# Kernel tuning notes

Measured on AMD Instinct MI355X. Metric: run time of the kernel, lower is better.

## Reference

```python
import jax, jax.numpy as jnp
import numpy as np

HIDDEN = 256
N_HEADS = 4
HEAD_DIM = HIDDEN // N_HEADS
SCALE = float(np.sqrt(HEAD_DIM))


def setup_inputs() -> dict:
    key = jax.random.key(0)
    ks = jax.random.split(key, 10)
    B, NQ, NKV = 2, 4096, 4096
    s = 1.0 / np.sqrt(HIDDEN)
    inp = {
        "query": jax.random.normal(ks[0], (B, NQ, HIDDEN), dtype=jnp.float32),
        "key_value": jax.random.normal(ks[1], (B, NKV, HIDDEN), dtype=jnp.float32),
        "kv_mask": jnp.ones((B, NKV), dtype=jnp.int32),
        "Wq": jax.random.uniform(ks[2], (HIDDEN, HIDDEN), jnp.float32, -s, s),
        "bq": jnp.zeros((HIDDEN,), jnp.float32),
        "Wk": jax.random.uniform(ks[3], (HIDDEN, HIDDEN), jnp.float32, -s, s),
        "bk": jnp.zeros((HIDDEN,), jnp.float32),
        "Wv": jax.random.uniform(ks[4], (HIDDEN, HIDDEN), jnp.float32, -s, s),
        "bv": jnp.zeros((HIDDEN,), jnp.float32),
        "Wo": jax.random.uniform(ks[5], (HIDDEN, HIDDEN), jnp.float32, -s, s),
        "bo": jnp.zeros((HIDDEN,), jnp.float32),
    }
    return inp


def reference(query, key_value, kv_mask, Wq, bq, Wk, bk, Wv, bv, Wo, bo):
    B, NQ, D = query.shape
    NKV = key_value.shape[1]
    # projections; reshape to (B, H, S, Dh)
    q = (query @ Wq + bq).reshape(B, NQ, N_HEADS, HEAD_DIM).transpose(0, 2, 1, 3)
    k = (key_value @ Wk + bk).reshape(B, NKV, N_HEADS, HEAD_DIM).transpose(0, 2, 1, 3)
    v = (key_value @ Wv + bv).reshape(B, NKV, N_HEADS, HEAD_DIM).transpose(0, 2, 1, 3)
    # scores: (B, H, NQ, NKV)
    attn = jnp.einsum("bhqd,bhkd->bhqk", q, k) / SCALE
    mask = (kv_mask != 0)[:, None, None, :]  # (B,1,1,NKV)
    attn = jnp.where(mask, attn, -jnp.inf)
    attn = jax.nn.softmax(attn, axis=-1)
    # dropout is identity in eval mode (reference is deterministic)
    out = jnp.einsum("bhqk,bhkd->bhqd", attn, v)
    out = out.transpose(0, 2, 1, 3).reshape(B, NQ, D)
    return out @ Wo + bo
```

## Files before the change

kernel.cpp:

```cpp
#include <hip/hip_runtime.h>
#include <hip/hip_bf16.h>
#include <math.h>

#define HID   256
#define NHEADS  4
#define HDIM   64
#define SEQ  4096
#define BATCH   2
#define MTOK (BATCH * SEQ)
#define LOG2E 1.44269504088896340736f
#define MFIX  8.0f

typedef short bf16x8 __attribute__((ext_vector_type(8)));
typedef float f32x4  __attribute__((ext_vector_type(4)));

__device__ __forceinline__ unsigned short f2b(float f) {
  union { float f; unsigned u; } v; v.f = f;
  return (unsigned short)((v.u + 0x7FFFu + ((v.u >> 16) & 1u)) >> 16);
}
__device__ __forceinline__ unsigned pkb(float a, float b) {
  __hip_bfloat162 h = __float22bfloat162_rn(make_float2(a, b));
  union { __hip_bfloat162 h; unsigned u; } v; v.h = h;
  return v.u;
}
__device__ __forceinline__ float exp2_(float x) {
#if __has_builtin(__builtin_amdgcn_exp2f)
  return __builtin_amdgcn_exp2f(x);
#else
  return exp2f(x);
#endif
}

__global__ __launch_bounds__(256)
void cast_wt(const float* __restrict__ W0, const float* __restrict__ W1,
             const float* __restrict__ W2, const float* __restrict__ W3,
             unsigned short* __restrict__ Wt) {
  __shared__ float t[64][65];
  const float* Ws[4] = {W0, W1, W2, W3};
  const float scl[4] = {0.125f * LOG2E, 1.f, 1.f, 1.f};
  const int wsel = blockIdx.y;
  const float* W = Ws[wsel];
  const float s = scl[wsel];
  unsigned short* O = Wt + (size_t)wsel * HID * HID;
  const int kt = (blockIdx.x & 3) * 64, nt = (blockIdx.x >> 2) * 64;
  const int tid = threadIdx.x;
#pragma unroll
  for (int p = 0; p < 4; ++p) {
    int i = p * 256 + tid;
    int r = i >> 4, c4 = (i & 15) * 4;
    *(float4*)&t[r][c4] = *(const float4*)&W[(size_t)(kt + r) * HID + nt + c4];
  }
  __syncthreads();
#pragma unroll
  for (int p = 0; p < 4; ++p) {
    int i = p * 256 + tid;
    int rn = i >> 4, ck = (i & 15) * 4;
    ushort4 o;
    o.x = f2b(t[ck + 0][rn] * s);
    o.y = f2b(t[ck + 1][rn] * s);
    o.z = f2b(t[ck + 2][rn] * s);
    o.w = f2b(t[ck + 3][rn] * s);
    *(ushort4*)&O[(size_t)(nt + rn) * HID + kt + ck] = o;
  }
}

__global__ __launch_bounds__(256)
void gemm_qkv(const float* __restrict__ query, const float* __restrict__ keyv,
              const unsigned short* __restrict__ wts,
              const float* __restrict__ bq, const float* __restrict__ bk,
              const float* __restrict__ bv,
              unsigned short* qp, unsigned short* kp, unsigned short* vtp) {
  __shared__ __align__(16) unsigned short As[2][64][136];
  __shared__ __align__(16) unsigned short Bs[64][136];
  float (*L)[68] = (float (*)[68])&Bs[0][0];

  const int tid = threadIdx.x;
  const int w = tid >> 6, lane = tid & 63, lq = lane & 15, quad = lane >> 4;
  const int wm = w & 1, wn = w >> 1;
  const int z = blockIdx.y;
  const int m0 = blockIdx.x * 64;

  const float* A = (z == 0) ? query : keyv;
  const unsigned short* Bt = wts + (size_t)z * HID * HID;
  const float* bias = (z == 0) ? bq : ((z == 1) ? bk : bv);
  const float bscale = (z == 0) ? 0.125f * LOG2E : 1.0f;

#pragma unroll
  for (int p = 0; p < 16; ++p) {
    int i = p * 256 + tid;
    int r = i >> 6, c4 = (i & 63) * 4;
    float4 f4 = *(const float4*)&A[(size_t)(m0 + r) * HID + c4];
    unsigned lo = pkb(f4.x, f4.y), hi = pkb(f4.z, f4.w);
    *(uint2*)&As[c4 >> 7][r][c4 & 127] = make_uint2(lo, hi);
  }
  __syncthreads();

  for (int n = 0; n < 4; ++n) {
    const int n0 = n * 64;
    f32x4 acc[2][2];
#pragma unroll
    for (int i = 0; i < 2; ++i)
#pragma unroll
      for (int j = 0; j < 2; ++j) acc[i][j] = (f32x4){0.f, 0.f, 0.f, 0.f};

#pragma unroll
    for (int kt = 0; kt < 2; ++kt) {
#pragma unroll
      for (int p = 0; p < 4; ++p) {
        int i = p * 256 + tid;
        int r = i >> 4, c8 = (i & 15) * 8;
        *(uint4*)&Bs[r][c8] =
            *(const uint4*)&Bt[(size_t)(n0 + r) * HID + kt * 128 + c8];
      }
      __syncthreads();
#pragma unroll
      for (int ks = 0; ks < 4; ++ks) {
        bf16x8 a0 = *(const bf16x8*)&As[kt][wm * 32 + lq][ks * 32 + quad * 8];
        bf16x8 a1 = *(const bf16x8*)&As[kt][wm * 32 + 16 + lq][ks * 32 + quad * 8];
        bf16x8 b0 = *(const bf16x8*)&Bs[wn * 32 + lq][ks * 32 + quad * 8];
        bf16x8 b1 = *(const bf16x8*)&Bs[wn * 32 + 16 + lq][ks * 32 + quad * 8];
        acc[0][0] = __builtin_amdgcn_mfma_f32_16x16x32_bf16(a0, b0, acc[0][0], 0, 0, 0);
        acc[0][1] = __builtin_amdgcn_mfma_f32_16x16x32_bf16(a0, b1, acc[0][1], 0, 0, 0);
        acc[1][0] = __builtin_amdgcn_mfma_f32_16x16x32_bf16(a1, b0, acc[1][0], 0, 0, 0);
        acc[1][1] = __builtin_amdgcn_mfma_f32_16x16x32_bf16(a1, b1, acc[1][1], 0, 0, 0);
      }
      __syncthreads();
    }

#pragma unroll
    for (int ni = 0; ni < 2; ++ni) {
      const float bv = bias[n0 + wn * 32 + ni * 16 + lq] * bscale;
#pragma unroll
      for (int mi = 0; mi < 2; ++mi)
#pragma unroll
        for (int r = 0; r < 4; ++r)
          L[wm * 32 + mi * 16 + quad * 4 + r][wn * 32 + ni * 16 + lq] =
              acc[mi][ni][r] + bv;
    }
    __syncthreads();

    if (z == 2) {
      const int nn = tid >> 2, mb4 = (tid & 3) * 16;
      __align__(16) unsigned short tmp[16];
#pragma unroll
      for (int j = 0; j < 16; ++j) {
        int p = mb4 + j;
        int k = ((p & 3) << 4) + (p >> 2);
        tmp[j] = f2b(L[k][nn]);
      }
      *(uint4*)&vtp[(size_t)(n0 + nn) * MTOK + m0 + mb4]     = *(uint4*)&tmp[0];
      *(uint4*)&vtp[(size_t)(n0 + nn) * MTOK + m0 + mb4 + 8] = *(uint4*)&tmp[8];
    } else {
      unsigned short* Y = (z == 0) ? qp : kp;
      const int r = tid >> 2, cb = (tid & 3) * 16;
      __align__(16) unsigned short tmp[16];
#pragma unroll
      for (int j = 0; j < 4; ++j) {
        float4 v4 = *(const float4*)&L[r][cb + j * 4];
        *(uint2*)&tmp[j * 4] = make_uint2(pkb(v4.x, v4.y), pkb(v4.z, v4.w));
      }
      *(uint4*)&Y[(size_t)(m0 + r) * HID + n0 + cb]     = *(uint4*)&tmp[0];
      *(uint4*)&Y[(size_t)(m0 + r) * HID + n0 + cb + 8] = *(uint4*)&tmp[8];
    }
    __syncthreads();
  }
}

__global__ __launch_bounds__(256)
void gemm_out(const unsigned short* __restrict__ ao,
              const unsigned short* __restrict__ wot,
              const float* __restrict__ bo, float* __restrict__ out) {
  __shared__ __align__(16) unsigned short As[64][136];
  __shared__ __align__(16) unsigned short Bs[64][136];
  float (*L)[68] = (float (*)[68])&As[0][0];

  const int tid = threadIdx.x;
  const int w = tid >> 6, lane = tid & 63, lq = lane & 15, quad = lane >> 4;
  const int wm = w & 1, wn = w >> 1;
  const int m0 = blockIdx.y * 64, n0 = blockIdx.x * 64;

  f32x4 acc[2][2];
#pragma unroll
  for (int i = 0; i < 2; ++i)
#pragma unroll
    for (int j = 0; j < 2; ++j) acc[i][j] = (f32x4){0.f, 0.f, 0.f, 0.f};

#pragma unroll
  for (int kt = 0; kt < 2; ++kt) {
    const int k0 = kt * 128;
#pragma unroll
    for (int p = 0; p < 4; ++p) {
      int i = p * 256 + tid;
      int r = i >> 4, c8 = (i & 15) * 8;
      *(uint4*)&As[r][c8] = *(const uint4*)&ao[(size_t)(m0 + r) * HID + k0 + c8];
      *(uint4*)&Bs[r][c8] = *(const uint4*)&wot[(size_t)(n0 + r) * HID + k0 + c8];
    }
    __syncthreads();
#pragma unroll
    for (int ks = 0; ks < 4; ++ks) {
      bf16x8 a0 = *(const bf16x8*)&As[wm * 32 + lq][ks * 32 + quad * 8];
      bf16x8 a1 = *(const bf16x8*)&As[wm * 32 + 16 + lq][ks * 32 + quad * 8];
      bf16x8 b0 = *(const bf16x8*)&Bs[wn * 32 + lq][ks * 32 + quad * 8];
      bf16x8 b1 = *(const bf16x8*)&Bs[wn * 32 + 16 + lq][ks * 32 + quad * 8];
      acc[0][0] = __builtin_amdgcn_mfma_f32_16x16x32_bf16(a0, b0, acc[0][0], 0, 0, 0);
      acc[0][1] = __builtin_amdgcn_mfma_f32_16x16x32_bf16(a0, b1, acc[0][1], 0, 0, 0);
      acc[1][0] = __builtin_amdgcn_mfma_f32_16x16x32_bf16(a1, b0, acc[1][0], 0, 0, 0);
      acc[1][1] = __builtin_amdgcn_mfma_f32_16x16x32_bf16(a1, b1, acc[1][1], 0, 0, 0);
    }
    __syncthreads();
  }

#pragma unroll
  for (int ni = 0; ni < 2; ++ni) {
    const float bv = bo[n0 + wn * 32 + ni * 16 + lq];
#pragma unroll
    for (int mi = 0; mi < 2; ++mi)
#pragma unroll
      for (int r = 0; r < 4; ++r)
        L[wm * 32 + mi * 16 + quad * 4 + r][wn * 32 + ni * 16 + lq] =
            acc[mi][ni][r] + bv;
  }
  __syncthreads();

  const int r = tid >> 2, cb = (tid & 3) * 16;
#pragma unroll
  for (int j = 0; j < 4; ++j) {
    float4 v4 = *(const float4*)&L[r][cb + j * 4];
    *(float4*)&out[(size_t)(m0 + r) * HID + n0 + cb + j * 4] = v4;
  }
}

__global__ __launch_bounds__(512, 2)
void flash_attn_mfma(const unsigned short* __restrict__ Qp,
                     const unsigned short* __restrict__ Kp,
                     const unsigned short* __restrict__ Vtp,
                     const int* __restrict__ mask,
                     unsigned short* __restrict__ Ao) {
  __shared__ __align__(16) unsigned short Ks[128][72];
  __shared__ __align__(16) unsigned short Vt[64][136];
  __shared__ __align__(16) unsigned short Ps[8][16][72];
  __shared__ float mb[128];

  const int tid = threadIdx.x;
  const int w = tid >> 6, lane = tid & 63, lq = lane & 15, quad = lane >> 4;
  const int bh = blockIdx.x;
  const int b = bh >> 2, h = bh & 3;
  const int q0 = blockIdx.y * 128;
  const int qbase = b * SEQ + q0, kvbase = b * SEQ, coff = h * HDIM;

  bf16x8 qf0, qf1;
  {
    const unsigned short* qr = &Qp[(size_t)(qbase + w * 16 + lq) * HID + coff + quad * 8];
    qf0 = *(const bf16x8*)&qr[0];
    qf1 = *(const bf16x8*)&qr[32];
  }

  const short oneb = (short)0x3F80;
  const bf16x8 ones = {oneb, oneb, oneb, oneb, oneb, oneb, oneb, oneb};

  f32x4 o[4], ls;
#pragma unroll
  for (int c = 0; c < 4; ++c) o[c] = (f32x4){0.f, 0.f, 0.f, 0.f};
  ls = (f32x4){0.f, 0.f, 0.f, 0.f};

  const int NT = SEQ / 128;
  for (int t = 0; t < NT; ++t) {
    const int k0 = t * 128;
#pragma unroll
    for (int p = 0; p < 2; ++p) {
      int idx = p * 512 + tid;
      int rk = idx >> 3, ck = (idx & 7) * 8;
      uint4 k4 = *(const uint4*)&Kp[(size_t)(kvbase + k0 + rk) * HID + coff + ck];
      int rv = idx >> 4, cv = (idx & 15) * 8;
      uint4 v4 = *(const uint4*)&Vtp[(size_t)(coff + rv) * MTOK + kvbase + k0 + cv];
      *(uint4*)&Ks[rk][ck] = k4;
      *(uint4*)&Vt[rv][cv] = v4;
    }
    if (tid < 128) mb[tid] = mask[kvbase + k0 + tid] ? -MFIX : -1e30f;
    __syncthreads();

    f32x4 sc[8];
#pragma unroll
    for (int c = 0; c < 8; ++c) {
      sc[c] = (f32x4){0.f, 0.f, 0.f, 0.f};
      bf16x8 kb0 = *(const bf16x8*)&Ks[c * 16 + lq][quad * 8];
      bf16x8 kb1 = *(const bf16x8*)&Ks[c * 16 + lq][32 + quad * 8];
      sc[c] = __builtin_amdgcn_mfma_f32_16x16x32_bf16(qf0, kb0, sc[c], 0, 0, 0);
      sc[c] = __builtin_amdgcn_mfma_f32_16x16x32_bf16(qf1, kb1, sc[c], 0, 0, 0);
    }
    float mbias[8];
#pragma unroll
    for (int c = 0; c < 8; ++c) mbias[c] = mb[c * 16 + lq];

#pragma unroll
    for (int hh = 0; hh < 2; ++hh) {
#pragma unroll
      for (int r = 0; r < 4; ++r) {
        const int row = quad * 4 + r;
        unsigned a0 = pkb(exp2_(sc[hh * 4 + 0][r] + mbias[hh * 4 + 0]),
                          exp2_(sc[hh * 4 + 1][r] + mbias[hh * 4 + 1]));
        unsigned a1 = pkb(exp2_(sc[hh * 4 + 2][r] + mbias[hh * 4 + 2]),
                          exp2_(sc[hh * 4 + 3][r] + mbias[hh * 4 + 3]));
        *(uint2*)&Ps[w][row][lq * 4] = make_uint2(a0, a1);
      }
#pragma unroll
      for (int i = 0; i < 2; ++i) {
        bf16x8 pa = *(const bf16x8*)&Ps[w][lq][i * 32 + quad * 8];
        ls = __builtin_amdgcn_mfma_f32_16x16x32_bf16(pa, ones, ls, 0, 0, 0);
#pragma unroll
        for (int c = 0; c < 4; ++c) {
          bf16x8 vb = *(const bf16x8*)&Vt[c * 16 + lq][hh * 64 + i * 32 + quad * 8];
          o[c] = __builtin_amdgcn_mfma_f32_16x16x32_bf16(pa, vb, o[c], 0, 0, 0);
        }
      }
    }
    __syncthreads();
  }

#pragma unroll
  for (int r = 0; r < 4; ++r) {
    float inv = 1.f / ls[r];
    const size_t row = (size_t)(qbase + w * 16 + quad * 4 + r);
#pragma unroll
    for (int c = 0; c < 4; ++c)
      Ao[row * HID + coff + c * 16 + lq] = f2b(o[c][r] * inv);
  }
}

extern "C" void kernel_launch(void* const* d_in, const int* in_sizes, int n_in,
                              void* d_out, int out_size, void* d_ws, size_t ws_size,
                              hipStream_t stream) {
  const float* query = (const float*)d_in[0];
  const float* keyv  = (const float*)d_in[1];
  const int*   mask  = (const int*)d_in[2];
  const float* Wq = (const float*)d_in[3];
  const float* bq = (const float*)d_in[4];
  const float* Wk = (const float*)d_in[5];
  const float* bk = (const float*)d_in[6];
  const float* Wv = (const float*)d_in[7];
  const float* bv = (const float*)d_in[8];
  const float* Wo = (const float*)d_in[9];
  const float* bo = (const float*)d_in[10];
  float* out = (float*)d_out;

  unsigned short* wts = (unsigned short*)d_ws;
  unsigned short* qp  = wts + (size_t)4 * HID * HID;
  unsigned short* kp  = qp  + (size_t)MTOK * HID;
  unsigned short* vtp = kp  + (size_t)MTOK * HID;
  unsigned short* ao  = vtp + (size_t)MTOK * HID;

  const unsigned short* wo_t = wts + 3 * HID * HID;

  dim3 blk(256);
  hipLaunchKernelGGL(cast_wt, dim3(16, 4), blk, 0, stream, Wq, Wk, Wv, Wo, wts);

  dim3 qkvgrid(MTOK / 64, 3);
  hipLaunchKernelGGL(gemm_qkv, qkvgrid, blk, 0, stream,
                     query, keyv, wts, bq, bk, bv, qp, kp, vtp);

  dim3 fgrid(BATCH * NHEADS, SEQ / 128);
  hipLaunchKernelGGL(flash_attn_mfma, fgrid, dim3(512), 0, stream,
                     qp, kp, vtp, mask, ao);

  dim3 ogrid(HID / 64, MTOK / 64);
  hipLaunchKernelGGL(gemm_out, ogrid, blk, 0, stream, ao, wo_t, bo, out);
}
```

Before: 175.9 us.

## Double-buffer K/V tiles in LDS with register prefetch in flash attention

Adds two LDS buffers for K, V^T and the mask bias. The next tile is loaded into registers at the start of each iteration and written to the alternate buffer after compute, so global-load latency overlaps the MFMA work and one barrier per iteration is removed. In exchange, LDS use roughly doubles, register pressure rises, and launch bounds drop to one block per SM, which may reduce occupancy.

```diff
diff --git a/kernel.cpp b/kernel.cpp
--- a/kernel.cpp
+++ b/kernel.cpp
@@ -230,16 +230,16 @@
   }
 }
 
-__global__ __launch_bounds__(512, 2)
+__global__ __launch_bounds__(512, 1)
 void flash_attn_mfma(const unsigned short* __restrict__ Qp,
                      const unsigned short* __restrict__ Kp,
                      const unsigned short* __restrict__ Vtp,
                      const int* __restrict__ mask,
                      unsigned short* __restrict__ Ao) {
-  __shared__ __align__(16) unsigned short Ks[128][72];
-  __shared__ __align__(16) unsigned short Vt[64][136];
+  __shared__ __align__(16) unsigned short Ks[2][128][72];
+  __shared__ __align__(16) unsigned short Vt[2][64][136];
   __shared__ __align__(16) unsigned short Ps[8][16][72];
-  __shared__ float mb[128];
+  __shared__ float mb[2][128];
 
   const int tid = threadIdx.x;
   const int w = tid >> 6, lane = tid & 63, lq = lane & 15, quad = lane >> 4;
@@ -248,6 +248,11 @@
   const int q0 = blockIdx.y * 128;
   const int qbase = b * SEQ + q0, kvbase = b * SEQ, coff = h * HDIM;
 
+  const int rk0 = tid >> 3,          ck0 = (tid & 7) * 8;
+  const int rk1 = (512 + tid) >> 3,  ck1 = ((512 + tid) & 7) * 8;
+  const int rv0 = tid >> 4,          cv0 = (tid & 15) * 8;
+  const int rv1 = (512 + tid) >> 4,  cv1 = ((512 + tid) & 15) * 8;
+
   bf16x8 qf0, qf1;
   {
     const unsigned short* qr = &Qp[(size_t)(qbase + w * 16 + lq) * HID + coff + quad * 8];
@@ -263,34 +268,47 @@
   for (int c = 0; c < 4; ++c) o[c] = (f32x4){0.f, 0.f, 0.f, 0.f};
   ls = (f32x4){0.f, 0.f, 0.f, 0.f};
 
+  {
+    *(uint4*)&Ks[0][rk0][ck0] =
+        *(const uint4*)&Kp[(size_t)(kvbase + rk0) * HID + coff + ck0];
+    *(uint4*)&Ks[0][rk1][ck1] =
+        *(const uint4*)&Kp[(size_t)(kvbase + rk1) * HID + coff + ck1];
+    *(uint4*)&Vt[0][rv0][cv0] =
+        *(const uint4*)&Vtp[(size_t)(coff + rv0) * MTOK + kvbase + cv0];
+    *(uint4*)&Vt[0][rv1][cv1] =
+        *(const uint4*)&Vtp[(size_t)(coff + rv1) * MTOK + kvbase + cv1];
+    if (tid < 128) mb[0][tid] = mask[kvbase + tid] ? -MFIX : -1e30f;
+  }
+  __syncthreads();
+
   const int NT = SEQ / 128;
   for (int t = 0; t < NT; ++t) {
-    const int k0 = t * 128;
-#pragma unroll
-    for (int p = 0; p < 2; ++p) {
-      int idx = p * 512 + tid;
-      int rk = idx >> 3, ck = (idx & 7) * 8;
-      uint4 k4 = *(const uint4*)&Kp[(size_t)(kvbase + k0 + rk) * HID + coff + ck];
-      int rv = idx >> 4, cv = (idx & 15) * 8;
-      uint4 v4 = *(const uint4*)&Vtp[(size_t)(coff + rv) * MTOK + kvbase + k0 + cv];
-      *(uint4*)&Ks[rk][ck] = k4;
-      *(uint4*)&Vt[rv][cv] = v4;
-    }
-    if (tid < 128) mb[tid] = mask[kvbase + k0 + tid] ? -MFIX : -1e30f;
-    __syncthreads();
+    const int cur = t & 1, nxt = cur ^ 1;
+    const bool pf = (t + 1 < NT);
+
+    uint4 kA, kB, vA, vB;
+    float mbr = 0.f;
+    if (pf) {
+      const int k0n = (t + 1) * 128;
+      kA = *(const uint4*)&Kp[(size_t)(kvbase + k0n + rk0) * HID + coff + ck0];
+      kB = *(const uint4*)&Kp[(size_t)(kvbase + k0n + rk1) * HID + coff + ck1];
+      vA = *(const uint4*)&Vtp[(size_t)(coff + rv0) * MTOK + kvbase + k0n + cv0];
+      vB = *(const uint4*)&Vtp[(size_t)(coff + rv1) * MTOK + kvbase + k0n + cv1];
+      if (tid < 128) mbr = mask[kvbase + k0n + tid] ? -MFIX : -1e30f;
+    }
 
     f32x4 sc[8];
 #pragma unroll
     for (int c = 0; c < 8; ++c) {
       sc[c] = (f32x4){0.f, 0.f, 0.f, 0.f};
-      bf16x8 kb0 = *(const bf16x8*)&Ks[c * 16 + lq][quad * 8];
-      bf16x8 kb1 = *(const bf16x8*)&Ks[c * 16 + lq][32 + quad * 8];
+      bf16x8 kb0 = *(const bf16x8*)&Ks[cur][c * 16 + lq][quad * 8];
+      bf16x8 kb1 = *(const bf16x8*)&Ks[cur][c * 16 + lq][32 + quad * 8];
       sc[c] = __builtin_amdgcn_mfma_f32_16x16x32_bf16(qf0, kb0, sc[c], 0, 0, 0);
       sc[c] = __builtin_amdgcn_mfma_f32_16x16x32_bf16(qf1, kb1, sc[c], 0, 0, 0);
     }
     float mbias[8];
 #pragma unroll
-    for (int c = 0; c < 8; ++c) mbias[c] = mb[c * 16 + lq];
+    for (int c = 0; c < 8; ++c) mbias[c] = mb[cur][c * 16 + lq];
 
 #pragma unroll
     for (int hh = 0; hh < 2; ++hh) {
@@ -309,10 +327,18 @@
         ls = __builtin_amdgcn_mfma_f32_16x16x32_bf16(pa, ones, ls, 0, 0, 0);
 #pragma unroll
         for (int c = 0; c < 4; ++c) {
-          bf16x8 vb = *(const bf16x8*)&Vt[c * 16 + lq][hh * 64 + i * 32 + quad * 8];
+          bf16x8 vb = *(const bf16x8*)&Vt[cur][c * 16 + lq][hh * 64 + i * 32 + quad * 8];
           o[c] = __builtin_amdgcn_mfma_f32_16x16x32_bf16(pa, vb, o[c], 0, 0, 0);
         }
       }
+    }
+
+    if (pf) {
+      *(uint4*)&Ks[nxt][rk0][ck0] = kA;
+      *(uint4*)&Ks[nxt][rk1][ck1] = kB;
+      *(uint4*)&Vt[nxt][rv0][cv0] = vA;
+      *(uint4*)&Vt[nxt][rv1][cv1] = vB;
+      if (tid < 128) mb[nxt][tid] = mbr;
     }
     __syncthreads();
   }
```

Result: faster. 161.5 us (-8.2%).
